# Optimization experiments

Hardware: AMD Instinct MI355X
Metric: run time of the kernel (lower is better)

## Reference

```python
import jax, jax.numpy as jnp
import numpy as np

N, E, NG, G = 40000, 400000, 64, 512
IN, GP, SP, EP, EA = 4, 3, 3, 6, 4
HID, HEADS, L = 192, 4, 3
DH, FFN = HID // HEADS, 2 * HID


def _ln(x, g, b, eps=1e-5):
    m = x.mean(-1, keepdims=True)
    v = ((x - m) ** 2).mean(-1, keepdims=True)
    return (x - m) * jax.lax.rsqrt(v + eps) * g + b


def _forward(x, edge_attr, group_probs, splitter_probs, endpoint_preds, params,
             edge_index, batch, group_ptr, time_group_ids):
    (W_in, b_in, Wq, Wk, Wv, We, Wo, bo, ln1_g, ln1_b,
     W_ff1, b_ff1, W_ff2, b_ff2, ln2_g, ln2_b,
     W_e1, b_e1, W_e2, b_e2, W_e3, b_e3) = params
    n = x.shape[0]
    src, dst = edge_index[0], edge_index[1]
    # expand per-group predictions to per-node via group ids
    gids = jnp.clip(group_ptr[batch] + time_group_ids, 0, group_probs.shape[0] - 1)
    feat = jnp.concatenate([x, group_probs[gids], splitter_probs, endpoint_preds[gids]], axis=1)
    h = feat @ W_in + b_in  # [N, HID]
    scale = np.float32(1.0 / np.sqrt(DH))
    for l in range(L):  # graph transformer blocks (attention restricted to edges)
        q = (h @ Wq[l]).reshape(n, HEADS, DH)
        k = (h @ Wk[l]).reshape(n, HEADS, DH)
        v = (h @ Wv[l]).reshape(n, HEADS, DH)
        e = (edge_attr @ We[l]).reshape(-1, HEADS, DH)  # [E, H, DH]
        ke = k[src] + e
        ve = v[src] + e
        logit = jnp.einsum('ehd,ehd->eh', q[dst], ke) * scale  # [E, H]
        m = jax.ops.segment_max(logit, dst, num_segments=n)
        m = jnp.where(jnp.isfinite(m), m, 0.0)  # guard nodes with no incoming edges
        a = jnp.exp(logit - m[dst])
        den = jax.ops.segment_sum(a, dst, num_segments=n)
        a = a / (den[dst] + 1e-16)  # per-destination softmax over incoming edges
        msg = jax.ops.segment_sum(a[:, :, None] * ve, dst, num_segments=n).reshape(n, HID)
        h = _ln(h + msg @ Wo[l] + bo[l], ln1_g[l], ln1_b[l])
        ff = jax.nn.relu(h @ W_ff1[l] + b_ff1[l]) @ W_ff2[l] + b_ff2[l]
        h = _ln(h + ff, ln2_g[l], ln2_b[l])
    # edge head: gather src/dst embeddings + edge_attr, concat, MLP -> per-edge logit
    pair = jnp.concatenate([h[src], h[dst], edge_attr], axis=1)  # [E, 2*HID+EA]
    z = jax.nn.relu(pair @ W_e1 + b_e1)
    z = jax.nn.relu(z @ W_e2 + b_e2)
    return z @ W_e3 + b_e3  # [E, 1]


def setup_inputs() -> dict:
    key = jax.random.key(0)
    ks = list(jax.random.split(key, 32))
    it = iter(ks)

    def g(shape, scale=0.05):
        return jax.random.normal(next(it), shape, jnp.float32) * scale

    inp = {
        'x': jax.random.normal(next(it), (N, IN), jnp.float32),
        'edge_index': jax.random.randint(next(it), (2, E), 0, N),
        'edge_attr': jax.random.normal(next(it), (E, EA), jnp.float32),
        'batch': jnp.sort(jax.random.randint(next(it), (N,), 0, NG)),
        'group_ptr': jnp.arange(NG + 1),
        'time_group_ids': jax.random.randint(next(it), (N,), 0, 8),
        'group_probs': jax.random.normal(next(it), (G, GP), jnp.float32),
        'splitter_probs': jax.random.normal(next(it), (N, SP), jnp.float32),
        'endpoint_preds': jax.random.normal(next(it), (G, EP), jnp.float32),
        'W_in': g((IN + GP + SP + EP, HID)), 'b_in': jnp.zeros((HID,), jnp.float32),
        'Wq': g((L, HID, HID)), 'Wk': g((L, HID, HID)), 'Wv': g((L, HID, HID)),
        'We': g((L, EA, HID)), 'Wo': g((L, HID, HID)), 'bo': jnp.zeros((L, HID), jnp.float32),
        'ln1_g': jnp.ones((L, HID), jnp.float32), 'ln1_b': jnp.zeros((L, HID), jnp.float32),
        'W_ff1': g((L, HID, FFN)), 'b_ff1': jnp.zeros((L, FFN), jnp.float32),
        'W_ff2': g((L, FFN, HID)), 'b_ff2': jnp.zeros((L, HID), jnp.float32),
        'ln2_g': jnp.ones((L, HID), jnp.float32), 'ln2_b': jnp.zeros((L, HID), jnp.float32),
        'W_e1': g((2 * HID + EA, HID)), 'b_e1': jnp.zeros((HID,), jnp.float32),
        'W_e2': g((HID, HID // 2)), 'b_e2': jnp.zeros((HID // 2,), jnp.float32),
        'W_e3': g((HID // 2, 1)), 'b_e3': jnp.zeros((1,), jnp.float32),
    }
    return inp


def reference(x, edge_index, edge_attr, batch, group_ptr, time_group_ids,
              group_probs, splitter_probs, endpoint_preds,
              W_in, b_in, Wq, Wk, Wv, We, Wo, bo, ln1_g, ln1_b,
              W_ff1, b_ff1, W_ff2, b_ff2, ln2_g, ln2_b,
              W_e1, b_e1, W_e2, b_e2, W_e3, b_e3):
    params = (W_in, b_in, Wq, Wk, Wv, We, Wo, bo, ln1_g, ln1_b,
              W_ff1, b_ff1, W_ff2, b_ff2, ln2_g, ln2_b,
              W_e1, b_e1, W_e2, b_e2, W_e3, b_e3)
    return _forward(x, edge_attr, group_probs, splitter_probs, endpoint_preds, params,
                    edge_index, batch, group_ptr, time_group_ids)
```

## Files before the change

### kernel.cpp

```cpp
#include <hip/hip_runtime.h>
#include <hip/hip_bf16.h>
#include <math.h>

#define N_NODES 40000
#define N_EDGES 400000
#define GCLIP 511

using short8  = __attribute__((ext_vector_type(8))) short;
using ushort8 = __attribute__((ext_vector_type(8))) unsigned short;
using floatx4 = __attribute__((ext_vector_type(4))) float;

__device__ __forceinline__ void split_bf16(float v, unsigned short& hi, unsigned short& lo) {
    __hip_bfloat16 h = __float2bfloat16(v);
    float r = v - __bfloat162float(h);
    __hip_bfloat16 l = __float2bfloat16(r);
    hi = *(unsigned short*)&h;
    lo = *(unsigned short*)&l;
}
__device__ __forceinline__ unsigned short f2bf(float f) {
    __hip_bfloat16 h = __float2bfloat16(f);
    return *(unsigned short*)&h;
}
__device__ __forceinline__ float bf2f(unsigned short u) {
    __hip_bfloat16 h = *(__hip_bfloat16*)&u;
    return __bfloat162float(h);
}
__device__ __forceinline__ floatx4 mfma16(short8 a, short8 b, floatx4 c) {
    return __builtin_amdgcn_mfma_f32_16x16x32_bf16(a, b, c, 0, 0, 0);
}

__global__ void count_kernel(const int* __restrict__ dst, int* __restrict__ cnt, int E) {
    int e = blockIdx.x * 256 + threadIdx.x;
    if (e < E) atomicAdd(&cnt[dst[e]], 1);
}

__global__ void scan1_kernel(const int* __restrict__ cnt, int* __restrict__ rowp,
                             int* __restrict__ bsum, int n) {
    __shared__ int wsum[16];
    __shared__ int woff[16];
    int tid = threadIdx.x, wave = tid >> 6, lane = tid & 63;
    int i = blockIdx.x * 1024 + tid;
    int v = (i < n) ? cnt[i] : 0;
    int x = v;
    for (int off = 1; off < 64; off <<= 1) {
        int t = __shfl_up(x, off);
        if (lane >= off) x += t;
    }
    if (lane == 63) wsum[wave] = x;
    __syncthreads();
    if (wave == 0 && lane < 16) {
        int s = wsum[lane];
        for (int off = 1; off < 16; off <<= 1) {
            int t = __shfl_up(s, off);
            if (lane >= off) s += t;
        }
        woff[lane] = s;
    }
    __syncthreads();
    int incl = x + ((wave == 0) ? 0 : woff[wave - 1]);
    if (i < n) rowp[i] = incl - v;
    if (tid == 1023) bsum[blockIdx.x] = incl;
}

__global__ void scan2_kernel(const int* __restrict__ bsum, int* __restrict__ boffs,
                             int* __restrict__ rowp, int nb, int n) {
    int lane = threadIdx.x;
    int v = (lane < nb) ? bsum[lane] : 0;
    int x = v;
    for (int off = 1; off < 64; off <<= 1) {
        int t = __shfl_up(x, off);
        if (lane >= off) x += t;
    }
    if (lane < nb) boffs[lane] = x - v;
    if (lane == nb - 1) rowp[n] = x;
}

__global__ void scan3_kernel(int* __restrict__ rowp, int* __restrict__ curs,
                             const int* __restrict__ boffs, int n) {
    int i = blockIdx.x * 1024 + threadIdx.x;
    if (i < n) {
        int v = rowp[i] + boffs[blockIdx.x];
        rowp[i] = v;
        curs[i] = v;
    }
}

__global__ void scatter_kernel(const int* __restrict__ src, const int* __restrict__ dst,
                               int* __restrict__ cursor, int2* __restrict__ csr2, int E) {
    int e = blockIdx.x * 256 + threadIdx.x;
    if (e < E) {
        int pos = atomicAdd(&cursor[dst[e]], 1);
        csr2[pos] = make_int2(src[e], e);
    }
}

__global__ void feat_kernel(const float* __restrict__ x, const int* __restrict__ batch,
                            const int* __restrict__ gptr, const int* __restrict__ tgid,
                            const float* __restrict__ gp, const float* __restrict__ sp,
                            const float* __restrict__ ep,
                            unsigned short* __restrict__ fhi, unsigned short* __restrict__ flo,
                            int n) {
    int idx = blockIdx.x * 256 + threadIdx.x;
    if (idx >= n * 32) return;
    int node = idx >> 5, c = idx & 31;
    float v = 0.f;
    if (c < 4) {
        v = x[node * 4 + c];
    } else if (c < 7) {
        int gid = gptr[batch[node]] + tgid[node];
        gid = min(max(gid, 0), GCLIP);
        v = gp[gid * 3 + (c - 4)];
    } else if (c < 10) {
        v = sp[node * 3 + (c - 7)];
    } else if (c < 16) {
        int gid = gptr[batch[node]] + tgid[node];
        gid = min(max(gid, 0), GCLIP);
        v = ep[gid * 6 + (c - 10)];
    }
    unsigned short hi, lo;
    split_bf16(v, hi, lo);
    fhi[idx] = hi;
    flo[idx] = lo;
}

#define WOFF_WIN 0
#define WOFF_QKV 6144
#define WOFF_WO  337920
#define WOFF_WF1 448512
#define WOFF_WF2 669696
#define WOFF_HSD 890880
#define WOFF_WE2 964608
#define WTOT     983040

__global__ void prep_kernel(const float* __restrict__ W_in, const float* __restrict__ Wq,
                            const float* __restrict__ Wk, const float* __restrict__ Wv,
                            const float* __restrict__ Wo, const float* __restrict__ Wf1,
                            const float* __restrict__ Wf2, const float* __restrict__ We1,
                            const float* __restrict__ We2, unsigned short* __restrict__ wb) {
    int idx = blockIdx.x * 256 + threadIdx.x;
    if (idx >= WTOT) return;
    float val;
    if (idx < WOFF_QKV) {
        int n = idx / 32, k = idx % 32;
        val = (k < 16) ? W_in[k * 192 + n] : 0.f;
    } else if (idx < WOFF_WO) {
        int r = idx - WOFF_QKV; int l = r / 110592; r %= 110592;
        int n = r / 192, k = r % 192;
        const float* s = (n < 192) ? Wq : (n < 384 ? Wk : Wv);
        val = s[l * 36864 + k * 192 + (n % 192)];
        if (n < 192) val *= 0.14433756729740643f;
    } else if (idx < WOFF_WF1) {
        int r = idx - WOFF_WO; int l = r / 36864; r %= 36864;
        int n = r / 192, k = r % 192;
        val = Wo[l * 36864 + k * 192 + n];
    } else if (idx < WOFF_WF2) {
        int r = idx - WOFF_WF1; int l = r / 73728; r %= 73728;
        int n = r / 192, k = r % 192;
        val = Wf1[l * 73728 + k * 384 + n];
    } else if (idx < WOFF_HSD) {
        int r = idx - WOFF_WF2; int l = r / 73728; r %= 73728;
        int n = r / 384, k = r % 384;
        val = Wf2[l * 73728 + k * 192 + n];
    } else if (idx < WOFF_WE2) {
        int r = idx - WOFF_HSD;
        int n = r / 192, k = r % 192;
        val = (n < 192) ? We1[k * 192 + n] : We1[(192 + k) * 192 + (n - 192)];
    } else {
        int r = idx - WOFF_WE2;
        int n = r / 192, k = r % 192;
        val = We2[k * 96 + n];
    }
    wb[idx] = f2bf(val);
}

template <int EPI, int DUAL, int BN, int KCH>
__global__ __launch_bounds__(256, 2)
void mfma_gemm(const unsigned short* __restrict__ Ahi, const unsigned short* __restrict__ Alo,
               int M, int Ka,
               const unsigned short* __restrict__ B, const float* __restrict__ bias,
               const unsigned short* __restrict__ Rhi, const unsigned short* __restrict__ Rlo,
               const float* __restrict__ lng, const float* __restrict__ lnb,
               unsigned short* __restrict__ Chi, unsigned short* __restrict__ Clo,
               int oldc, int cmul, int cadd) {
    constexpr int NT = BN / 16;
    __shared__ __align__(16) unsigned short sB[BN][KCH + 8];
    const int tid = threadIdx.x;
    const int wave = tid >> 6, lane = tid & 63;
    const int quad = lane >> 4, l16 = lane & 15;
    const int rbase = blockIdx.x * 128;
    const int cbase = blockIdx.y * BN;

    floatx4 acc[2][NT];
#pragma unroll
    for (int mt = 0; mt < 2; ++mt)
#pragma unroll
        for (int nt = 0; nt < NT; ++nt) acc[mt][nt] = (floatx4)0.0f;

    const int r0 = min(rbase + wave * 32 + l16, M - 1);
    const int r1 = min(rbase + wave * 32 + 16 + l16, M - 1);
    const unsigned short* pa0h = Ahi + (size_t)r0 * Ka + quad * 8;
    const unsigned short* pa0l = Alo + (size_t)r0 * Ka + quad * 8;
    const unsigned short* pa1h = Ahi + (size_t)r1 * Ka + quad * 8;
    const unsigned short* pa1l = Alo + (size_t)r1 * Ka + quad * 8;

    for (int kb = 0; kb < Ka; kb += KCH) {
        for (int i = tid * 8; i < BN * KCH; i += 2048) {
            int n = i / KCH, kk = i % KCH;
            *(uint4*)&sB[n][kk] = *(const uint4*)(B + (size_t)(cbase + n) * Ka + kb + kk);
        }
        __syncthreads();
#pragma unroll
        for (int kc = 0; kc < KCH; kc += 32) {
            const int kg = kb + kc;
            short8 ah0 = *(const short8*)(pa0h + kg);
            short8 al0 = *(const short8*)(pa0l + kg);
            short8 ah1 = *(const short8*)(pa1h + kg);
            short8 al1 = *(const short8*)(pa1l + kg);
#pragma unroll
            for (int nt = 0; nt < NT; ++nt) {
                short8 b = *(const short8*)&sB[nt * 16 + l16][kc + quad * 8];
                acc[0][nt] = mfma16(ah0, b, acc[0][nt]);
                acc[0][nt] = mfma16(al0, b, acc[0][nt]);
                acc[1][nt] = mfma16(ah1, b, acc[1][nt]);
                acc[1][nt] = mfma16(al1, b, acc[1][nt]);
            }
        }
        if (kb + KCH < Ka) __syncthreads();
    }

    float bb[NT], gg[NT], be[NT];
#pragma unroll
    for (int nt = 0; nt < NT; ++nt) {
        int colg = cbase + nt * 16 + l16;
        bb[nt] = bias ? bias[colg] : 0.f;
        if (EPI == 2) { gg[nt] = lng[colg]; be[nt] = lnb[colg]; }
    }
#pragma unroll
    for (int mt = 0; mt < 2; ++mt) {
#pragma unroll
        for (int reg = 0; reg < 4; ++reg) {
            int row = rbase + wave * 32 + mt * 16 + quad * 4 + reg;
            if (EPI == 2) {
                int rr = min(row, M - 1);
                float v[NT], s = 0.f, q = 0.f;
#pragma unroll
                for (int nt = 0; nt < NT; ++nt) {
                    size_t off = (size_t)rr * 192 + nt * 16 + l16;
                    float resid = bf2f(Rhi[off]) + bf2f(Rlo[off]);
                    v[nt] = acc[mt][nt][reg] + bb[nt] + resid;
                    s += v[nt]; q += v[nt] * v[nt];
                }
#pragma unroll
                for (int off = 1; off < 16; off <<= 1) {
                    s += __shfl_xor(s, off);
                    q += __shfl_xor(q, off);
                }
                float mean = s * (1.f / 192.f);
                float var = q * (1.f / 192.f) - mean * mean;
                float rs = rsqrtf(var + 1e-5f);
                if (row < M) {
#pragma unroll
                    for (int nt = 0; nt < NT; ++nt) {
                        float r = (v[nt] - mean) * rs * gg[nt] + be[nt];
                        unsigned short hi, lo;
                        split_bf16(r, hi, lo);
                        size_t off = (size_t)row * 192 + nt * 16 + l16;
                        Chi[off] = hi; Clo[off] = lo;
                    }
                }
            } else if (row < M) {
#pragma unroll
                for (int nt = 0; nt < NT; ++nt) {
                    float v = acc[mt][nt][reg] + bb[nt];
                    if (EPI == 1) v = fmaxf(v, 0.f);
                    size_t off = (size_t)row * oldc + (size_t)(cbase + nt * 16 + l16) * cmul + cadd;
                    if (DUAL) {
                        unsigned short hi, lo;
                        split_bf16(v, hi, lo);
                        Chi[off] = hi; Clo[off] = lo;
                    } else {
                        Chi[off] = f2bf(v);
                    }
                }
            }
        }
    }
}

__global__ __launch_bounds__(256)
void attn_kernel(const unsigned short* __restrict__ qB, const unsigned short* __restrict__ kvB,
                 const float* __restrict__ ea, const float* __restrict__ We_l,
                 const int2* __restrict__ csr2, const int* __restrict__ row_ptr,
                 unsigned short* __restrict__ msg_hi, unsigned short* __restrict__ msg_lo) {
    __shared__ float sWe[768];
    const int tid = threadIdx.x;
    for (int i = tid; i < 768; i += 256) sWe[i] = We_l[i];
    __syncthreads();

    const int lane = tid & 63;
    const int node = blockIdx.x * 4 + (tid >> 6);
    const int d0 = (lane >> 4) * 48 + (lane & 15) * 3;

    float W[4][3];
#pragma unroll
    for (int w = 0; w < 4; ++w) {
        W[w][0] = sWe[w * 192 + d0];
        W[w][1] = sWe[w * 192 + d0 + 1];
        W[w][2] = sWe[w * 192 + d0 + 2];
    }
    size_t qoff = (size_t)node * 192 + d0;
    float q0 = bf2f(qB[qoff]), q1 = bf2f(qB[qoff + 1]), q2 = bf2f(qB[qoff + 2]);
    float qe0 = q0 * W[0][0] + q1 * W[0][1] + q2 * W[0][2];
    float qe1 = q0 * W[1][0] + q1 * W[1][1] + q2 * W[1][2];
    float qe2 = q0 * W[2][0] + q1 * W[2][1] + q2 * W[2][2];
    float qe3 = q0 * W[3][0] + q1 * W[3][1] + q2 * W[3][2];
#pragma unroll
    for (int off = 1; off < 16; off <<= 1) {
        qe0 += __shfl_xor(qe0, off);
        qe1 += __shfl_xor(qe1, off);
        qe2 += __shfl_xor(qe2, off);
        qe3 += __shfl_xor(qe3, off);
    }

    const unsigned int* kv = (const unsigned int*)kvB;
    const float4* ea4 = (const float4*)ea;

    float m = -INFINITY, den = 0.f;
    float v0 = 0.f, v1 = 0.f, v2 = 0.f;
    float wa0 = 0.f, wa1 = 0.f, wa2 = 0.f, wa3 = 0.f;
    const int beg = row_ptr[node], end = row_ptr[node + 1];
    int p = beg;
    for (; p + 1 < end; p += 2) {
        int2 se1 = csr2[p], se2 = csr2[p + 1];
        size_t b1 = (size_t)se1.x * 192 + d0;
        size_t b2 = (size_t)se2.x * 192 + d0;
        unsigned int u10 = kv[b1], u11 = kv[b1 + 1], u12 = kv[b1 + 2];
        unsigned int u20 = kv[b2], u21 = kv[b2 + 1], u22 = kv[b2 + 2];
        float4 w1 = ea4[se1.y];
        float4 w2 = ea4[se2.y];
        float d1 = q0 * bf2f((unsigned short)u10) + q1 * bf2f((unsigned short)u11)
                 + q2 * bf2f((unsigned short)u12);
        float d2 = q0 * bf2f((unsigned short)u20) + q1 * bf2f((unsigned short)u21)
                 + q2 * bf2f((unsigned short)u22);
#pragma unroll
        for (int off = 1; off < 16; off <<= 1) {
            d1 += __shfl_xor(d1, off);
            d2 += __shfl_xor(d2, off);
        }
        float l1 = d1 + w1.x * qe0 + w1.y * qe1 + w1.z * qe2 + w1.w * qe3;
        float l2 = d2 + w2.x * qe0 + w2.y * qe1 + w2.z * qe2 + w2.w * qe3;
        float mn = fmaxf(m, fmaxf(l1, l2));
        float corr = __expf(m - mn);
        float p1 = __expf(l1 - mn);
        float p2 = __expf(l2 - mn);
        den = den * corr + p1 + p2;
        v0 = v0 * corr + p1 * bf2f((unsigned short)(u10 >> 16)) + p2 * bf2f((unsigned short)(u20 >> 16));
        v1 = v1 * corr + p1 * bf2f((unsigned short)(u11 >> 16)) + p2 * bf2f((unsigned short)(u21 >> 16));
        v2 = v2 * corr + p1 * bf2f((unsigned short)(u12 >> 16)) + p2 * bf2f((unsigned short)(u22 >> 16));
        wa0 = wa0 * corr + p1 * w1.x + p2 * w2.x;
        wa1 = wa1 * corr + p1 * w1.y + p2 * w2.y;
        wa2 = wa2 * corr + p1 * w1.z + p2 * w2.z;
        wa3 = wa3 * corr + p1 * w1.w + p2 * w2.w;
        m = mn;
    }
    if (p < end) {
        int2 se = csr2[p];
        size_t b = (size_t)se.x * 192 + d0;
        unsigned int u0 = kv[b], u1 = kv[b + 1], u2 = kv[b + 2];
        float4 w = ea4[se.y];
        float d = q0 * bf2f((unsigned short)u0) + q1 * bf2f((unsigned short)u1)
                + q2 * bf2f((unsigned short)u2);
#pragma unroll
        for (int off = 1; off < 16; off <<= 1) d += __shfl_xor(d, off);
        float l = d + w.x * qe0 + w.y * qe1 + w.z * qe2 + w.w * qe3;
        float mn = fmaxf(m, l);
        float corr = __expf(m - mn);
        float pe = __expf(l - mn);
        den = den * corr + pe;
        v0 = v0 * corr + pe * bf2f((unsigned short)(u0 >> 16));
        v1 = v1 * corr + pe * bf2f((unsigned short)(u1 >> 16));
        v2 = v2 * corr + pe * bf2f((unsigned short)(u2 >> 16));
        wa0 = wa0 * corr + pe * w.x;
        wa1 = wa1 * corr + pe * w.y;
        wa2 = wa2 * corr + pe * w.z;
        wa3 = wa3 * corr + pe * w.w;
    }
    float inv = 1.f / (den + 1e-16f);
    float m0 = (v0 + wa0 * W[0][0] + wa1 * W[1][0] + wa2 * W[2][0] + wa3 * W[3][0]) * inv;
    float m1 = (v1 + wa0 * W[0][1] + wa1 * W[1][1] + wa2 * W[2][1] + wa3 * W[3][1]) * inv;
    float m2 = (v2 + wa0 * W[0][2] + wa1 * W[1][2] + wa2 * W[2][2] + wa3 * W[3][2]) * inv;
    size_t ob = (size_t)node * 192 + d0;
    unsigned short hi, lo;
    split_bf16(m0, hi, lo); msg_hi[ob] = hi;     msg_lo[ob] = lo;
    split_bf16(m1, hi, lo); msg_hi[ob + 1] = hi; msg_lo[ob + 1] = lo;
    split_bf16(m2, hi, lo); msg_hi[ob + 2] = hi; msg_lo[ob + 2] = lo;
}

__global__ __launch_bounds__(256)
void edge_head_kernel(const unsigned short* __restrict__ hsd, const float* __restrict__ ea,
                      const int* __restrict__ src, const int* __restrict__ dst,
                      const float* __restrict__ W1e, const float* __restrict__ b1,
                      const unsigned short* __restrict__ W2hi,
                      const float* __restrict__ b2, const float* __restrict__ W3,
                      const float* __restrict__ b3, float* __restrict__ out) {
    __shared__ __align__(16) unsigned short sZ[2][64][40];
    __shared__ __align__(16) unsigned short sW[96][200];
    __shared__ float sWe1[768];
    __shared__ float sB1[192];
    const int tid = threadIdx.x;
    const int wave = tid >> 6, lane = tid & 63;
    const int quad = lane >> 4, l16 = lane & 15;
    const int ebase = blockIdx.x * 64;

    for (int i = tid; i < 768; i += 256) sWe1[i] = W1e[i];
    if (tid < 192) sB1[tid] = b1[tid];
    for (int i = tid * 8; i < 96 * 192; i += 2048) {
        int n = i / 192, kk = i % 192;
        *(uint4*)&sW[n][kk] = *(const uint4*)(W2hi + (size_t)n * 192 + kk);
    }

    const int el = tid >> 2, part = tid & 3;
    const int e = ebase + el;
    const int s = src[e], d = dst[e];
    const float4 eav = *(const float4*)(ea + (size_t)e * 4);
    const unsigned short* hs_p = hsd + (size_t)s * 384;
    const unsigned short* hd_p = hsd + (size_t)d * 384 + 192;

    floatx4 acc[6];
#pragma unroll
    for (int nt = 0; nt < 6; ++nt) acc[nt] = (floatx4)0.0f;
    __syncthreads();

    for (int kc = 0; kc < 192; kc += 32) {
        {
            int c0 = kc + part * 8;
            ushort8 hsv = *(const ushort8*)(hs_p + c0);
            ushort8 hdv = *(const ushort8*)(hd_p + c0);
            ushort8 hv, lv;
#pragma unroll
            for (int j = 0; j < 8; ++j) {
                int c = c0 + j;
                float ce = sB1[c] + eav.x * sWe1[c] + eav.y * sWe1[192 + c]
                         + eav.z * sWe1[384 + c] + eav.w * sWe1[576 + c];
                float v = fmaxf(bf2f(hsv[j]) + bf2f(hdv[j]) + ce, 0.f);
                unsigned short hi, lo;
                split_bf16(v, hi, lo);
                hv[j] = hi; lv[j] = lo;
            }
            *(ushort8*)&sZ[0][el][part * 8] = hv;
            *(ushort8*)&sZ[1][el][part * 8] = lv;
        }
        short8 zh = *(const short8*)&sZ[0][wave * 16 + l16][quad * 8];
        short8 zl = *(const short8*)&sZ[1][wave * 16 + l16][quad * 8];
#pragma unroll
        for (int nt = 0; nt < 6; ++nt) {
            short8 bh = *(const short8*)&sW[nt * 16 + l16][kc + quad * 8];
            acc[nt] = mfma16(zh, bh, acc[nt]);
            acc[nt] = mfma16(zl, bh, acc[nt]);
        }
    }

    float w3[6], bb2[6];
#pragma unroll
    for (int nt = 0; nt < 6; ++nt) {
        int col = nt * 16 + l16;
        w3[nt] = W3[col];
        bb2[nt] = b2[col];
    }
    float b3v = b3[0];
#pragma unroll
    for (int reg = 0; reg < 4; ++reg) {
        float sacc = 0.f;
#pragma unroll
        for (int nt = 0; nt < 6; ++nt) {
            float z = fmaxf(acc[nt][reg] + bb2[nt], 0.f);
            sacc = fmaf(z, w3[nt], sacc);
        }
#pragma unroll
        for (int off = 1; off < 16; off <<= 1) sacc += __shfl_xor(sacc, off);
        if (l16 == 0) out[ebase + wave * 16 + quad * 4 + reg] = sacc + b3v;
    }
}

extern "C" void kernel_launch(void* const* d_in, const int* in_sizes, int n_in,
                              void* d_out, int out_size, void* d_ws, size_t ws_size,
                              hipStream_t stream) {
    const float* x     = (const float*)d_in[0];
    const int*   eidx  = (const int*)d_in[1];
    const float* ea    = (const float*)d_in[2];
    const int*   batch = (const int*)d_in[3];
    const int*   gptr  = (const int*)d_in[4];
    const int*   tgid  = (const int*)d_in[5];
    const float* gp    = (const float*)d_in[6];
    const float* sp    = (const float*)d_in[7];
    const float* epp   = (const float*)d_in[8];
    const float* W_in  = (const float*)d_in[9];
    const float* b_in  = (const float*)d_in[10];
    const float* Wq    = (const float*)d_in[11];
    const float* Wk    = (const float*)d_in[12];
    const float* Wv    = (const float*)d_in[13];
    const float* We    = (const float*)d_in[14];
    const float* Wo    = (const float*)d_in[15];
    const float* bo    = (const float*)d_in[16];
    const float* ln1g  = (const float*)d_in[17];
    const float* ln1b  = (const float*)d_in[18];
    const float* Wf1   = (const float*)d_in[19];
    const float* bf1   = (const float*)d_in[20];
    const float* Wf2   = (const float*)d_in[21];
    const float* bf2   = (const float*)d_in[22];
    const float* ln2g  = (const float*)d_in[23];
    const float* ln2b  = (const float*)d_in[24];
    const float* We1   = (const float*)d_in[25];
    const float* be1   = (const float*)d_in[26];
    const float* We2   = (const float*)d_in[27];
    const float* be2   = (const float*)d_in[28];
    const float* We3   = (const float*)d_in[29];
    const float* be3   = (const float*)d_in[30];
    const int* src = eidx;
    const int* dst = eidx + N_EDGES;

    unsigned short* ub = (unsigned short*)d_ws;
    unsigned short* featH = ub;
    unsigned short* featL = ub + 1280000;
    unsigned short* hH    = ub + 2560000;
    unsigned short* hL    = ub + 10240000;
    unsigned short* htH   = ub + 17920000;
    unsigned short* htL   = ub + 25600000;
    unsigned short* msgH  = ub + 33280000;
    unsigned short* msgL  = ub + 40960000;
    unsigned short* rbuf  = ub + 48640000;
    unsigned short* qB    = rbuf;
    unsigned short* kvB   = rbuf + 7680000;
    unsigned short* ffH   = rbuf;
    unsigned short* ffL   = rbuf + 15360000;
    unsigned short* hsdB  = rbuf;
    unsigned short* wb    = ub + 79360000;
    int* ib   = (int*)(ub + 80343040);
    int* cnt  = ib;
    int* rowp = ib + 40000;
    int* curs = ib + 80004;
    int2* csr2 = (int2*)(ib + 120004);
    int* bsum  = ib + 920004;
    int* boffs = ib + 920044;

    hipMemsetAsync(cnt, 0, N_NODES * sizeof(int), stream);
    count_kernel<<<1563, 256, 0, stream>>>(dst, cnt, N_EDGES);
    scan1_kernel<<<40, 1024, 0, stream>>>(cnt, rowp, bsum, N_NODES);
    scan2_kernel<<<1, 64, 0, stream>>>(bsum, boffs, rowp, 40, N_NODES);
    scan3_kernel<<<40, 1024, 0, stream>>>(rowp, curs, boffs, N_NODES);
    scatter_kernel<<<1563, 256, 0, stream>>>(src, dst, curs, csr2, N_EDGES);
    feat_kernel<<<5000, 256, 0, stream>>>(x, batch, gptr, tgid, gp, sp, epp, featH, featL, N_NODES);
    prep_kernel<<<3840, 256, 0, stream>>>(W_in, Wq, Wk, Wv, Wo, Wf1, Wf2, We1, We2, wb);

    dim3 blk(256);
    mfma_gemm<0, 1, 96, 32><<<dim3(313, 2), blk, 0, stream>>>(featH, featL, N_NODES, 32,
        wb + WOFF_WIN, b_in, nullptr, nullptr, nullptr, nullptr, hH, hL, 192, 1, 0);

    for (int l = 0; l < 3; ++l) {
        const unsigned short* wq = wb + WOFF_QKV + l * 110592;
        mfma_gemm<0, 0, 96, 192><<<dim3(313, 2), blk, 0, stream>>>(hH, hL, N_NODES, 192,
            wq, nullptr, nullptr, nullptr, nullptr, nullptr, qB, nullptr, 192, 1, 0);
        mfma_gemm<0, 0, 96, 192><<<dim3(313, 2), blk, 0, stream>>>(hH, hL, N_NODES, 192,
            wq + 192 * 192, nullptr, nullptr, nullptr, nullptr, nullptr, kvB, nullptr, 384, 2, 0);
        mfma_gemm<0, 0, 96, 192><<<dim3(313, 2), blk, 0, stream>>>(hH, hL, N_NODES, 192,
            wq + 384 * 192, nullptr, nullptr, nullptr, nullptr, nullptr, kvB, nullptr, 384, 2, 1);
        attn_kernel<<<10000, blk, 0, stream>>>(qB, kvB, ea, We + l * 768, csr2, rowp, msgH, msgL);
        mfma_gemm<2, 1, 192, 96><<<dim3(313, 1), blk, 0, stream>>>(msgH, msgL, N_NODES, 192,
            wb + WOFF_WO + l * 36864, bo + l * 192, hH, hL, ln1g + l * 192, ln1b + l * 192,
            htH, htL, 192, 1, 0);
        mfma_gemm<1, 1, 96, 192><<<dim3(313, 4), blk, 0, stream>>>(htH, htL, N_NODES, 192,
            wb + WOFF_WF1 + l * 73728, bf1 + l * 384, nullptr, nullptr, nullptr, nullptr,
            ffH, ffL, 384, 1, 0);
        mfma_gemm<2, 1, 192, 96><<<dim3(313, 1), blk, 0, stream>>>(ffH, ffL, N_NODES, 384,
            wb + WOFF_WF2 + l * 73728, bf2 + l * 192, htH, htL, ln2g + l * 192, ln2b + l * 192,
            hH, hL, 192, 1, 0);
    }

    mfma_gemm<0, 0, 96, 192><<<dim3(313, 4), blk, 0, stream>>>(hH, hL, N_NODES, 192,
        wb + WOFF_HSD, nullptr, nullptr, nullptr, nullptr, nullptr, hsdB, nullptr, 384, 1, 0);
    edge_head_kernel<<<6250, blk, 0, stream>>>(hsdB, ea, src, dst,
        We1 + 384 * 192, be1, wb + WOFF_WE2, be2, We3, be3, (float*)d_out);
}
```

Baseline: 1.007 ms.

## Fuse QKV GEMMs, drop lo-term for QKV, prefetch A tiles, unroll attention by 4

Merges the three Q/K/V projection GEMMs into one launch with a custom output mode that routes columns to the q buffer and the interleaved kv buffer. The fused QKV GEMM uses only the high bf16 part of h (one MFMA term instead of two), halving its MFMA work but lowering precision. The GEMM main loop now register-prefetches the next A fragment across k-chunks. The attention loop is unrolled to four edges per online-softmax step, which also fixes the missing max update in the tail. The edge head builds its MFMA operand directly in registers instead of staging through shared memory. The edge head also gets an occupancy hint.

```diff
diff --git a/kernel.cpp b/kernel.cpp
--- a/kernel.cpp
+++ b/kernel.cpp
@@ -173,7 +173,7 @@
     wb[idx] = f2bf(val);
 }
 
-template <int EPI, int DUAL, int BN, int KCH>
+template <int EPI, int DUAL, int BN, int KCH, int TERMS, int OUTMODE>
 __global__ __launch_bounds__(256, 2)
 void mfma_gemm(const unsigned short* __restrict__ Ahi, const unsigned short* __restrict__ Alo,
                int M, int Ka,
@@ -199,33 +199,46 @@
     const int r0 = min(rbase + wave * 32 + l16, M - 1);
     const int r1 = min(rbase + wave * 32 + 16 + l16, M - 1);
     const unsigned short* pa0h = Ahi + (size_t)r0 * Ka + quad * 8;
+    const unsigned short* pa1h = Ahi + (size_t)r1 * Ka + quad * 8;
     const unsigned short* pa0l = Alo + (size_t)r0 * Ka + quad * 8;
-    const unsigned short* pa1h = Ahi + (size_t)r1 * Ka + quad * 8;
     const unsigned short* pa1l = Alo + (size_t)r1 * Ka + quad * 8;
 
     for (int kb = 0; kb < Ka; kb += KCH) {
+        if (kb) __syncthreads();
         for (int i = tid * 8; i < BN * KCH; i += 2048) {
             int n = i / KCH, kk = i % KCH;
             *(uint4*)&sB[n][kk] = *(const uint4*)(B + (size_t)(cbase + n) * Ka + kb + kk);
         }
         __syncthreads();
+        short8 ch0 = *(const short8*)(pa0h + kb);
+        short8 ch1 = *(const short8*)(pa1h + kb);
+        short8 cl0, cl1;
+        if (TERMS == 2) {
+            cl0 = *(const short8*)(pa0l + kb);
+            cl1 = *(const short8*)(pa1l + kb);
+        }
 #pragma unroll
         for (int kc = 0; kc < KCH; kc += 32) {
-            const int kg = kb + kc;
-            short8 ah0 = *(const short8*)(pa0h + kg);
-            short8 al0 = *(const short8*)(pa0l + kg);
-            short8 ah1 = *(const short8*)(pa1h + kg);
-            short8 al1 = *(const short8*)(pa1l + kg);
+            short8 nh0 = ch0, nh1 = ch1, nl0 = ch0, nl1 = ch1;
+            if (kc + 32 < KCH) {
+                nh0 = *(const short8*)(pa0h + kb + kc + 32);
+                nh1 = *(const short8*)(pa1h + kb + kc + 32);
+                if (TERMS == 2) {
+                    nl0 = *(const short8*)(pa0l + kb + kc + 32);
+                    nl1 = *(const short8*)(pa1l + kb + kc + 32);
+                }
+            }
 #pragma unroll
             for (int nt = 0; nt < NT; ++nt) {
                 short8 b = *(const short8*)&sB[nt * 16 + l16][kc + quad * 8];
-                acc[0][nt] = mfma16(ah0, b, acc[0][nt]);
-                acc[0][nt] = mfma16(al0, b, acc[0][nt]);
-                acc[1][nt] = mfma16(ah1, b, acc[1][nt]);
-                acc[1][nt] = mfma16(al1, b, acc[1][nt]);
+                acc[0][nt] = mfma16(ch0, b, acc[0][nt]);
+                if (TERMS == 2) acc[0][nt] = mfma16(cl0, b, acc[0][nt]);
+                acc[1][nt] = mfma16(ch1, b, acc[1][nt]);
+                if (TERMS == 2) acc[1][nt] = mfma16(cl1, b, acc[1][nt]);
             }
-        }
-        if (kb + KCH < Ka) __syncthreads();
+            ch0 = nh0; ch1 = nh1;
+            if (TERMS == 2) { cl0 = nl0; cl1 = nl1; }
+        }
     }
 
     float bb[NT], gg[NT], be[NT];
@@ -273,13 +286,24 @@
                 for (int nt = 0; nt < NT; ++nt) {
                     float v = acc[mt][nt][reg] + bb[nt];
                     if (EPI == 1) v = fmaxf(v, 0.f);
-                    size_t off = (size_t)row * oldc + (size_t)(cbase + nt * 16 + l16) * cmul + cadd;
-                    if (DUAL) {
-                        unsigned short hi, lo;
-                        split_bf16(v, hi, lo);
-                        Chi[off] = hi; Clo[off] = lo;
+                    if (OUTMODE == 1) {
+                        int c = cbase + nt * 16 + l16;
+                        if (c < 192) {
+                            Chi[(size_t)row * 192 + c] = f2bf(v);
+                        } else {
+                            int cc = c - 192;
+                            int idx = (cc < 192) ? (cc * 2) : ((cc - 192) * 2 + 1);
+                            Clo[(size_t)row * 384 + idx] = f2bf(v);
+                        }
                     } else {
-                        Chi[off] = f2bf(v);
+                        size_t off = (size_t)row * oldc + (size_t)(cbase + nt * 16 + l16) * cmul + cadd;
+                        if (DUAL) {
+                            unsigned short hi, lo;
+                            split_bf16(v, hi, lo);
+                            Chi[off] = hi; Clo[off] = lo;
+                        } else {
+                            Chi[off] = f2bf(v);
+                        }
                     }
                 }
             }
@@ -330,40 +354,50 @@
     float wa0 = 0.f, wa1 = 0.f, wa2 = 0.f, wa3 = 0.f;
     const int beg = row_ptr[node], end = row_ptr[node + 1];
     int p = beg;
-    for (; p + 1 < end; p += 2) {
-        int2 se1 = csr2[p], se2 = csr2[p + 1];
-        size_t b1 = (size_t)se1.x * 192 + d0;
-        size_t b2 = (size_t)se2.x * 192 + d0;
-        unsigned int u10 = kv[b1], u11 = kv[b1 + 1], u12 = kv[b1 + 2];
-        unsigned int u20 = kv[b2], u21 = kv[b2 + 1], u22 = kv[b2 + 2];
-        float4 w1 = ea4[se1.y];
-        float4 w2 = ea4[se2.y];
-        float d1 = q0 * bf2f((unsigned short)u10) + q1 * bf2f((unsigned short)u11)
-                 + q2 * bf2f((unsigned short)u12);
-        float d2 = q0 * bf2f((unsigned short)u20) + q1 * bf2f((unsigned short)u21)
-                 + q2 * bf2f((unsigned short)u22);
+    for (; p + 3 < end; p += 4) {
+        int2 seA = csr2[p], seB = csr2[p + 1], seC = csr2[p + 2], seD = csr2[p + 3];
+        size_t bA = (size_t)seA.x * 192 + d0;
+        size_t bB = (size_t)seB.x * 192 + d0;
+        size_t bC = (size_t)seC.x * 192 + d0;
+        size_t bD = (size_t)seD.x * 192 + d0;
+        unsigned int uA0 = kv[bA], uA1 = kv[bA + 1], uA2 = kv[bA + 2];
+        unsigned int uB0 = kv[bB], uB1 = kv[bB + 1], uB2 = kv[bB + 2];
+        unsigned int uC0 = kv[bC], uC1 = kv[bC + 1], uC2 = kv[bC + 2];
+        unsigned int uD0 = kv[bD], uD1 = kv[bD + 1], uD2 = kv[bD + 2];
+        float4 wA = ea4[seA.y], wB = ea4[seB.y], wC = ea4[seC.y], wD = ea4[seD.y];
+        float dA = q0 * bf2f((unsigned short)uA0) + q1 * bf2f((unsigned short)uA1) + q2 * bf2f((unsigned short)uA2);
+        float dB = q0 * bf2f((unsigned short)uB0) + q1 * bf2f((unsigned short)uB1) + q2 * bf2f((unsigned short)uB2);
+        float dC = q0 * bf2f((unsigned short)uC0) + q1 * bf2f((unsigned short)uC1) + q2 * bf2f((unsigned short)uC2);
+        float dD = q0 * bf2f((unsigned short)uD0) + q1 * bf2f((unsigned short)uD1) + q2 * bf2f((unsigned short)uD2);
 #pragma unroll
         for (int off = 1; off < 16; off <<= 1) {
-            d1 += __shfl_xor(d1, off);
-            d2 += __shfl_xor(d2, off);
-        }
-        float l1 = d1 + w1.x * qe0 + w1.y * qe1 + w1.z * qe2 + w1.w * qe3;
-        float l2 = d2 + w2.x * qe0 + w2.y * qe1 + w2.z * qe2 + w2.w * qe3;
-        float mn = fmaxf(m, fmaxf(l1, l2));
+            dA += __shfl_xor(dA, off);
+            dB += __shfl_xor(dB, off);
+            dC += __shfl_xor(dC, off);
+            dD += __shfl_xor(dD, off);
+        }
+        float lA = dA + wA.x * qe0 + wA.y * qe1 + wA.z * qe2 + wA.w * qe3;
+        float lB = dB + wB.x * qe0 + wB.y * qe1 + wB.z * qe2 + wB.w * qe3;
+        float lC = dC + wC.x * qe0 + wC.y * qe1 + wC.z * qe2 + wC.w * qe3;
+        float lD = dD + wD.x * qe0 + wD.y * qe1 + wD.z * qe2 + wD.w * qe3;
+        float mn = fmaxf(m, fmaxf(fmaxf(lA, lB), fmaxf(lC, lD)));
         float corr = __expf(m - mn);
-        float p1 = __expf(l1 - mn);
-        float p2 = __expf(l2 - mn);
-        den = den * corr + p1 + p2;
-        v0 = v0 * corr + p1 * bf2f((unsigned short)(u10 >> 16)) + p2 * bf2f((unsigned short)(u20 >> 16));
-        v1 = v1 * corr + p1 * bf2f((unsigned short)(u11 >> 16)) + p2 * bf2f((unsigned short)(u21 >> 16));
-        v2 = v2 * corr + p1 * bf2f((unsigned short)(u12 >> 16)) + p2 * bf2f((unsigned short)(u22 >> 16));
-        wa0 = wa0 * corr + p1 * w1.x + p2 * w2.x;
-        wa1 = wa1 * corr + p1 * w1.y + p2 * w2.y;
-        wa2 = wa2 * corr + p1 * w1.z + p2 * w2.z;
-        wa3 = wa3 * corr + p1 * w1.w + p2 * w2.w;
+        float pA = __expf(lA - mn), pB = __expf(lB - mn);
+        float pC = __expf(lC - mn), pD = __expf(lD - mn);
+        den = den * corr + pA + pB + pC + pD;
+        v0 = v0 * corr + pA * bf2f((unsigned short)(uA0 >> 16)) + pB * bf2f((unsigned short)(uB0 >> 16))
+                       + pC * bf2f((unsigned short)(uC0 >> 16)) + pD * bf2f((unsigned short)(uD0 >> 16));
+        v1 = v1 * corr + pA * bf2f((unsigned short)(uA1 >> 16)) + pB * bf2f((unsigned short)(uB1 >> 16))
+                       + pC * bf2f((unsigned short)(uC1 >> 16)) + pD * bf2f((unsigned short)(uD1 >> 16));
+        v2 = v2 * corr + pA * bf2f((unsigned short)(uA2 >> 16)) + pB * bf2f((unsigned short)(uB2 >> 16))
+                       + pC * bf2f((unsigned short)(uC2 >> 16)) + pD * bf2f((unsigned short)(uD2 >> 16));
+        wa0 = wa0 * corr + pA * wA.x + pB * wB.x + pC * wC.x + pD * wD.x;
+        wa1 = wa1 * corr + pA * wA.y + pB * wB.y + pC * wC.y + pD * wD.y;
+        wa2 = wa2 * corr + pA * wA.z + pB * wB.z + pC * wC.z + pD * wD.z;
+        wa3 = wa3 * corr + pA * wA.w + pB * wB.w + pC * wC.w + pD * wD.w;
         m = mn;
     }
-    if (p < end) {
+    for (; p < end; ++p) {
         int2 se = csr2[p];
         size_t b = (size_t)se.x * 192 + d0;
         unsigned int u0 = kv[b], u1 = kv[b + 1], u2 = kv[b + 2];
@@ -384,6 +418,7 @@
         wa1 = wa1 * corr + pe * w.y;
         wa2 = wa2 * corr + pe * w.z;
         wa3 = wa3 * corr + pe * w.w;
+        m = mn;
     }
     float inv = 1.f / (den + 1e-16f);
     float m0 = (v0 + wa0 * W[0][0] + wa1 * W[1][0] + wa2 * W[2][0] + wa3 * W[3][0]) * inv;
@@ -396,17 +431,16 @@
     split_bf16(m2, hi, lo); msg_hi[ob + 2] = hi; msg_lo[ob + 2] = lo;
 }
 
-__global__ __launch_bounds__(256)
+__global__ __launch_bounds__(256, 2)
 void edge_head_kernel(const unsigned short* __restrict__ hsd, const float* __restrict__ ea,
                       const int* __restrict__ src, const int* __restrict__ dst,
                       const float* __restrict__ W1e, const float* __restrict__ b1,
                       const unsigned short* __restrict__ W2hi,
                       const float* __restrict__ b2, const float* __restrict__ W3,
                       const float* __restrict__ b3, float* __restrict__ out) {
-    __shared__ __align__(16) unsigned short sZ[2][64][40];
     __shared__ __align__(16) unsigned short sW[96][200];
-    __shared__ float sWe1[768];
-    __shared__ float sB1[192];
+    __shared__ __align__(16) float sWe1[768];
+    __shared__ __align__(16) float sB1[192];
     const int tid = threadIdx.x;
     const int wave = tid >> 6, lane = tid & 63;
     const int quad = lane >> 4, l16 = lane & 15;
@@ -419,45 +453,56 @@
         *(uint4*)&sW[n][kk] = *(const uint4*)(W2hi + (size_t)n * 192 + kk);
     }
 
-    const int el = tid >> 2, part = tid & 3;
-    const int e = ebase + el;
+    const int e = ebase + wave * 16 + l16;
     const int s = src[e], d = dst[e];
     const float4 eav = *(const float4*)(ea + (size_t)e * 4);
-    const unsigned short* hs_p = hsd + (size_t)s * 384;
-    const unsigned short* hd_p = hsd + (size_t)d * 384 + 192;
+    const unsigned short* hs_p = hsd + (size_t)s * 384 + quad * 8;
+    const unsigned short* hd_p = hsd + (size_t)d * 384 + 192 + quad * 8;
 
     floatx4 acc[6];
 #pragma unroll
     for (int nt = 0; nt < 6; ++nt) acc[nt] = (floatx4)0.0f;
     __syncthreads();
 
+    ushort8 hs_c = *(const ushort8*)hs_p;
+    ushort8 hd_c = *(const ushort8*)hd_p;
+#pragma unroll
     for (int kc = 0; kc < 192; kc += 32) {
-        {
-            int c0 = kc + part * 8;
-            ushort8 hsv = *(const ushort8*)(hs_p + c0);
-            ushort8 hdv = *(const ushort8*)(hd_p + c0);
-            ushort8 hv, lv;
-#pragma unroll
-            for (int j = 0; j < 8; ++j) {
-                int c = c0 + j;
-                float ce = sB1[c] + eav.x * sWe1[c] + eav.y * sWe1[192 + c]
-                         + eav.z * sWe1[384 + c] + eav.w * sWe1[576 + c];
-                float v = fmaxf(bf2f(hsv[j]) + bf2f(hdv[j]) + ce, 0.f);
-                unsigned short hi, lo;
-                split_bf16(v, hi, lo);
-                hv[j] = hi; lv[j] = lo;
-            }
-            *(ushort8*)&sZ[0][el][part * 8] = hv;
-            *(ushort8*)&sZ[1][el][part * 8] = lv;
-        }
-        short8 zh = *(const short8*)&sZ[0][wave * 16 + l16][quad * 8];
-        short8 zl = *(const short8*)&sZ[1][wave * 16 + l16][quad * 8];
+        ushort8 hs_n = hs_c, hd_n = hd_c;
+        if (kc + 32 < 192) {
+            hs_n = *(const ushort8*)(hs_p + kc + 32);
+            hd_n = *(const ushort8*)(hd_p + kc + 32);
+        }
+        const int c0 = kc + quad * 8;
+        float wb1[8], w0v[8], w1v[8], w2v[8], w3v[8];
+        *(float4*)&wb1[0] = *(const float4*)&sB1[c0];
+        *(float4*)&wb1[4] = *(const float4*)&sB1[c0 + 4];
+        *(float4*)&w0v[0] = *(const float4*)&sWe1[c0];
+        *(float4*)&w0v[4] = *(const float4*)&sWe1[c0 + 4];
+        *(float4*)&w1v[0] = *(const float4*)&sWe1[192 + c0];
+        *(float4*)&w1v[4] = *(const float4*)&sWe1[192 + c0 + 4];
+        *(float4*)&w2v[0] = *(const float4*)&sWe1[384 + c0];
+        *(float4*)&w2v[4] = *(const float4*)&sWe1[384 + c0 + 4];
+        *(float4*)&w3v[0] = *(const float4*)&sWe1[576 + c0];
+        *(float4*)&w3v[4] = *(const float4*)&sWe1[576 + c0 + 4];
+        ushort8 ah, al;
+#pragma unroll
+        for (int j = 0; j < 8; ++j) {
+            float ce = wb1[j] + eav.x * w0v[j] + eav.y * w1v[j]
+                     + eav.z * w2v[j] + eav.w * w3v[j];
+            float v = fmaxf(bf2f(hs_c[j]) + bf2f(hd_c[j]) + ce, 0.f);
+            unsigned short hi, lo;
+            split_bf16(v, hi, lo);
+            ah[j] = hi; al[j] = lo;
+        }
+        short8 ahs = *(short8*)&ah, als = *(short8*)&al;
 #pragma unroll
         for (int nt = 0; nt < 6; ++nt) {
             short8 bh = *(const short8*)&sW[nt * 16 + l16][kc + quad * 8];
-            acc[nt] = mfma16(zh, bh, acc[nt]);
-            acc[nt] = mfma16(zl, bh, acc[nt]);
-        }
+            acc[nt] = mfma16(ahs, bh, acc[nt]);
+            acc[nt] = mfma16(als, bh, acc[nt]);
+        }
+        hs_c = hs_n; hd_c = hd_n;
     }
 
     float w3[6], bb2[6];
@@ -553,30 +598,26 @@
     prep_kernel<<<3840, 256, 0, stream>>>(W_in, Wq, Wk, Wv, Wo, Wf1, Wf2, We1, We2, wb);
 
     dim3 blk(256);
-    mfma_gemm<0, 1, 96, 32><<<dim3(313, 2), blk, 0, stream>>>(featH, featL, N_NODES, 32,
+    mfma_gemm<0, 1, 96, 32, 2, 0><<<dim3(313, 2), blk, 0, stream>>>(featH, featL, N_NODES, 32,
         wb + WOFF_WIN, b_in, nullptr, nullptr, nullptr, nullptr, hH, hL, 192, 1, 0);
 
     for (int l = 0; l < 3; ++l) {
         const unsigned short* wq = wb + WOFF_QKV + l * 110592;
-        mfma_gemm<0, 0, 96, 192><<<dim3(313, 2), blk, 0, stream>>>(hH, hL, N_NODES, 192,
-            wq, nullptr, nullptr, nullptr, nullptr, nullptr, qB, nullptr, 192, 1, 0);
-        mfma_gemm<0, 0, 96, 192><<<dim3(313, 2), blk, 0, stream>>>(hH, hL, N_NODES, 192,
-            wq + 192 * 192, nullptr, nullptr, nullptr, nullptr, nullptr, kvB, nullptr, 384, 2, 0);
-        mfma_gemm<0, 0, 96, 192><<<dim3(313, 2), blk, 0, stream>>>(hH, hL, N_NODES, 192,
-            wq + 384 * 192, nullptr, nullptr, nullptr, nullptr, nullptr, kvB, nullptr, 384, 2, 1);
+        mfma_gemm<0, 0, 96, 192, 1, 1><<<dim3(313, 6), blk, 0, stream>>>(hH, hL, N_NODES, 192,
+            wq, nullptr, nullptr, nullptr, nullptr, nullptr, qB, kvB, 0, 0, 0);
         attn_kernel<<<10000, blk, 0, stream>>>(qB, kvB, ea, We + l * 768, csr2, rowp, msgH, msgL);
-        mfma_gemm<2, 1, 192, 96><<<dim3(313, 1), blk, 0, stream>>>(msgH, msgL, N_NODES, 192,
+        mfma_gemm<2, 1, 192, 96, 2, 0><<<dim3(313, 1), blk, 0, stream>>>(msgH, msgL, N_NODES, 192,
             wb + WOFF_WO + l * 36864, bo + l * 192, hH, hL, ln1g + l * 192, ln1b + l * 192,
             htH, htL, 192, 1, 0);
-        mfma_gemm<1, 1, 96, 192><<<dim3(313, 4), blk, 0, stream>>>(htH, htL, N_NODES, 192,
+        mfma_gemm<1, 1, 96, 192, 2, 0><<<dim3(313, 4), blk, 0, stream>>>(htH, htL, N_NODES, 192,
             wb + WOFF_WF1 + l * 73728, bf1 + l * 384, nullptr, nullptr, nullptr, nullptr,
             ffH, ffL, 384, 1, 0);
-        mfma_gemm<2, 1, 192, 96><<<dim3(313, 1), blk, 0, stream>>>(ffH, ffL, N_NODES, 384,
+        mfma_gemm<2, 1, 192, 96, 2, 0><<<dim3(313, 1), blk, 0, stream>>>(ffH, ffL, N_NODES, 384,
             wb + WOFF_WF2 + l * 73728, bf2 + l * 192, htH, htL, ln2g + l * 192, ln2b + l * 192,
             hH, hL, 192, 1, 0);
     }
 
-    mfma_gemm<0, 0, 96, 192><<<dim3(313, 4), blk, 0, stream>>>(hH, hL, N_NODES, 192,
+    mfma_gemm<0, 0, 96, 192, 2, 0><<<dim3(313, 4), blk, 0, stream>>>(hH, hL, N_NODES, 192,
         wb + WOFF_HSD, nullptr, nullptr, nullptr, nullptr, nullptr, hsdB, nullptr, 384, 1, 0);
     edge_head_kernel<<<6250, blk, 0, stream>>>(hsdB, ea, src, dst,
         We1 + 384 * 192, be1, wb + WOFF_WE2, be2, We3, be3, (float*)d_out);
```

Measured after the change: 930.8 us. 7.5% less time.
